# Kernel tuning notes

Measured on AMD Instinct MI355X. Metric: run time of the kernel, lower is better.

## Reference

```python
import jax, jax.numpy as jnp
import numpy as np

N, E, G = 100000, 1600000, 512
D_IN, D_H, D_OUT = 128, 128, 1
EPS = 1e-5


def _gcn_conv(x, W, b, src, dst, n):
    # PyG GCNConv: h = x @ W, add self-loops, symmetric-normalized sum aggregation, bias after.
    h = x @ W
    loop = jnp.arange(n)
    s = jnp.concatenate([src, loop])
    d = jnp.concatenate([dst, loop])
    deg = jax.ops.segment_sum(jnp.ones(s.shape[0], dtype=h.dtype), d, num_segments=n)
    dinv = jnp.where(deg > 0, jax.lax.rsqrt(deg), 0.0)
    norm = dinv[s] * dinv[d]  # [E+N]
    out = jax.ops.segment_sum(h[s] * norm[:, None], d, num_segments=n)
    return out + b


def _bn(x, g, b, m, v):
    # eval-mode BatchNorm1d
    return (x - m) * jax.lax.rsqrt(v + EPS) * g + b


def setup_inputs() -> dict:
    key = jax.random.key(0)
    ks = jax.random.split(key, 24)
    x = jax.random.normal(ks[0], (N, D_IN), dtype=jnp.float32)
    edge_index = jax.random.randint(ks[1], (2, E), 0, N, dtype=jnp.int64)
    batch = (jnp.arange(N, dtype=jnp.int64) * G) // N  # sorted, all graphs non-empty
    inp = {"x": x, "edge_index": edge_index, "batch": batch}
    dims = [(D_IN, D_H), (D_H, D_H), (D_H, D_H)]
    for i, (din, dout) in enumerate(dims):
        sc = 1.0 / np.sqrt(din)
        inp[f"W{i}"] = jax.random.normal(ks[2 + 4 * i], (din, dout), dtype=jnp.float32) * sc
        inp[f"cb{i}"] = jnp.zeros((dout,), dtype=jnp.float32)
        inp[f"g{i}"] = jnp.ones((dout,), dtype=jnp.float32)
        inp[f"bt{i}"] = jnp.zeros((dout,), dtype=jnp.float32)
        inp[f"m{i}"] = jax.random.normal(ks[3 + 4 * i], (dout,), dtype=jnp.float32) * 0.1
        inp[f"v{i}"] = jax.random.uniform(ks[4 + 4 * i], (dout,), dtype=jnp.float32, minval=0.5, maxval=1.5)
    inp["L1w"] = jax.random.normal(ks[15], (2 * D_H, D_H), dtype=jnp.float32) / np.sqrt(2 * D_H)
    inp["L1b"] = jnp.zeros((D_H,), dtype=jnp.float32)
    inp["L2w"] = jax.random.normal(ks[16], (D_H, D_H // 2), dtype=jnp.float32) / np.sqrt(D_H)
    inp["L2b"] = jnp.zeros((D_H // 2,), dtype=jnp.float32)
    inp["L3w"] = jax.random.normal(ks[17], (D_H // 2, D_OUT), dtype=jnp.float32) / np.sqrt(D_H // 2)
    inp["L3b"] = jnp.zeros((D_OUT,), dtype=jnp.float32)
    return inp


def reference(x, edge_index, batch,
              W0, cb0, g0, bt0, m0, v0,
              W1, cb1, g1, bt1, m1, v1,
              W2, cb2, g2, bt2, m2, v2,
              L1w, L1b, L2w, L2b, L3w, L3b):
    src, dst = edge_index[0], edge_index[1]
    Ws = [W0, W1, W2]
    cbs = [cb0, cb1, cb2]
    bns = [(g0, bt0, m0, v0), (g1, bt1, m1, v1), (g2, bt2, m2, v2)]
    for i in range(3):
        x_prev = x
        x = _gcn_conv(x, Ws[i], cbs[i], src, dst, N)
        x = jax.nn.relu(_bn(x, *bns[i]))
        # dropout is identity in eval mode
        if i > 0:
            x = x + x_prev  # residual (shapes match for i > 0)
    ones = jnp.ones((N,), dtype=x.dtype)
    cnt = jax.ops.segment_sum(ones, batch, num_segments=G)[:, None]
    x_mean = jax.ops.segment_sum(x, batch, num_segments=G) / cnt
    x_max = jax.ops.segment_max(x, batch, num_segments=G)
    h = jnp.concatenate([x_mean, x_max], axis=1)  # [G, 2*D_H]
    h = jax.nn.relu(h @ L1w + L1b)
    h = jax.nn.relu(h @ L2w + L2b)
    return h @ L3w + L3b  # [G, 1]
```

## Files before the change

kernel.cpp:

```cpp
#include <hip/hip_runtime.h>
#include <math.h>

#define DH 128
#define EPSB 1e-5f
#define MAXB 832
#define BCAP 2560
#define LDAP 136

typedef __attribute__((ext_vector_type(8))) short short8;
typedef __attribute__((ext_vector_type(4))) float f32x4;

static __device__ __forceinline__ unsigned short f2bf(float f) {
    unsigned u = __float_as_uint(f);
    u += 0x7fffu + ((u >> 16) & 1u);
    return (unsigned short)(u >> 16);
}
static __device__ __forceinline__ float bf2f(unsigned short h) {
    return __uint_as_float(((unsigned)h) << 16);
}
static __device__ __forceinline__ float blo(unsigned u) { return __uint_as_float(u << 16); }
static __device__ __forceinline__ float bhi(unsigned u) { return __uint_as_float(u & 0xFFFF0000u); }


__launch_bounds__(256)
__global__ void k_bucketA(const int* __restrict__ src, const int* __restrict__ dst,
                          int* __restrict__ gcur, int* __restrict__ bbuf,
                          const int* __restrict__ batch, int* __restrict__ starts,
                          const float* __restrict__ W0, const float* __restrict__ W1,
                          const float* __restrict__ W2, unsigned short* __restrict__ Wf0,
                          int E, int NB, int chunk, int N, int G)
{
    const int t = threadIdx.x;

    if (blockIdx.x >= 512) {
        int fid = (blockIdx.x - 512) * 4 + (t >> 6);
        int lane = t & 63;
        int l = fid >> 6, f = fid & 63;
        const float* W = (l == 0) ? W0 : (l == 1) ? W1 : W2;
        unsigned short* Wf = Wf0 + (size_t)l * 32768;
        int nt = f & 3, s = (f >> 2) & 3, p = (f >> 4) & 1, nh = f >> 5;
        int n = nh * 64 + nt * 16 + (lane & 15);
        int kbase = s * 32 + (lane >> 4) * 8;
        unsigned short o[8];
#pragma unroll
        for (int j = 0; j < 8; ++j) {
            float w = W[(size_t)(kbase + j) * DH + n];
            unsigned short h = f2bf(w);
            o[j] = p ? f2bf(w - bf2f(h)) : h;
        }
        unsigned short* d = Wf + (size_t)f * 512 + lane * 8;
        *(ushort4*)d       = make_ushort4(o[0], o[1], o[2], o[3]);
        *(ushort4*)(d + 4) = make_ushort4(o[4], o[5], o[6], o[7]);
        return;
    }

    __shared__ int cnt[MAXB];
    __shared__ int base[MAXB];

    for (int i = blockIdx.x * 256 + t; i < N; i += 512 * 256) {
        int b = batch[i];
        if (i == 0) { starts[0] = 0; starts[G] = N; }
        else if (batch[i - 1] != b) starts[b] = i;
    }

    for (int i = t; i < NB; i += 256) cnt[i] = 0;
    __syncthreads();
    const int e0 = blockIdx.x * chunk;
    const int e1 = min(E, e0 + chunk);
    for (int e = e0 + t; e < e1; e += 256)
        atomicAdd(&cnt[dst[e] >> 7], 1);
    __syncthreads();
    for (int i = t; i < NB; i += 256) {
        int c = cnt[i];
        base[i] = (c > 0) ? atomicAdd(&gcur[i], c) : 0;
        cnt[i] = 0;
    }
    __syncthreads();
    for (int e = e0 + t; e < e1; e += 256) {
        int d = dst[e];
        int b = d >> 7;
        int o = base[b] + atomicAdd(&cnt[b], 1);
        if (o < BCAP) bbuf[(size_t)b * BCAP + o] = (src[e] << 7) | (d & 127);
    }
}


__launch_bounds__(256)
__global__ void k_bfinal(const int* __restrict__ gcur, int* __restrict__ bbuf,
                         int2* __restrict__ rowinfo, float* __restrict__ dinv, int N)
{
    __shared__ int ebuf[BCAP];
    __shared__ int dcnt[128];
    __shared__ int sp[128];
    const int b = blockIdx.x, t = threadIdx.x;
    const int c = min(gcur[b], BCAP);
    const int base = b * BCAP;
    int* p = bbuf + base;
    for (int i = t; i < c; i += 256) ebuf[i] = p[i];
    if (t < 128) dcnt[t] = 0;
    __syncthreads();
    for (int i = t; i < c; i += 256) atomicAdd(&dcnt[ebuf[i] & 127], 1);
    __syncthreads();
    if (t < 128) sp[t] = dcnt[t];
    __syncthreads();
    for (int off = 1; off < 128; off <<= 1) {
        int u = (t < 128 && t >= off) ? sp[t - off] : 0;
        __syncthreads();
        if (t < 128) sp[t] += u;
        __syncthreads();
    }
    if (t < 128) {
        sp[t] -= dcnt[t];
        int d = b * 128 + t;
        if (d < N) {
            rowinfo[d] = make_int2(base + sp[t], base + sp[t] + dcnt[t]);
            dinv[d] = rsqrtf((float)(dcnt[t] + 1));
        }
        dcnt[t] = 0;
    }
    __syncthreads();
    for (int i = t; i < c; i += 256) {
        int e = ebuf[i];
        int dl = e & 127;
        int o = atomicAdd(&dcnt[dl], 1);
        p[sp[dl] + o] = e >> 7;
    }
}


__launch_bounds__(256)
__global__ void k_gemm0(const float* __restrict__ X,
                        const unsigned short* __restrict__ Wf,
                        const float* __restrict__ dinv,
                        unsigned short* __restrict__ hs, int N)
{
    __shared__ unsigned short Ah[16 * 512];
    __shared__ unsigned short Al[16 * 512];

    const int tid  = threadIdx.x;
    const int lane = tid & 63, wave = tid >> 6;
    const int mh = wave >> 1, nh = wave & 1;
    const int rowBase = blockIdx.x * 64;
    const int r15 = lane & 15, quad = lane >> 4;

    {
        const int gl = tid >> 4;
        const int f8 = (tid & 15) * 8;
        const int s  = f8 >> 5;
        const int q  = (f8 >> 3) & 3;
        const int lp = q * 16 + gl;
#pragma unroll
        for (int it = 0; it < 4; ++it) {
            int row = rowBase + it * 16 + gl;
            float v[8];
            if (row < N) {
                float4 a0 = *(const float4*)(X + (size_t)row * DH + f8);
                float4 a1 = *(const float4*)(X + (size_t)row * DH + f8 + 4);
                v[0] = a0.x; v[1] = a0.y; v[2] = a0.z; v[3] = a0.w;
                v[4] = a1.x; v[5] = a1.y; v[6] = a1.z; v[7] = a1.w;
            } else {
#pragma unroll
                for (int j = 0; j < 8; ++j) v[j] = 0.f;
            }
            unsigned short hA[8], lA[8];
#pragma unroll
            for (int j = 0; j < 8; ++j) {
                unsigned short h = f2bf(v[j]);
                hA[j] = h; lA[j] = f2bf(v[j] - bf2f(h));
            }
            int reg = it * 4 + s;
            *(ushort4*)(Ah + reg * 512 + lp * 8)     = make_ushort4(hA[0], hA[1], hA[2], hA[3]);
            *(ushort4*)(Ah + reg * 512 + lp * 8 + 4) = make_ushort4(hA[4], hA[5], hA[6], hA[7]);
            *(ushort4*)(Al + reg * 512 + lp * 8)     = make_ushort4(lA[0], lA[1], lA[2], lA[3]);
            *(ushort4*)(Al + reg * 512 + lp * 8 + 4) = make_ushort4(lA[4], lA[5], lA[6], lA[7]);
        }
    }
    __syncthreads();

    f32x4 acc[2][4];
#pragma unroll
    for (int mt = 0; mt < 2; ++mt)
#pragma unroll
        for (int nt = 0; nt < 4; ++nt)
            acc[mt][nt] = (f32x4){0.f, 0.f, 0.f, 0.f};

#pragma unroll
    for (int s = 0; s < 4; ++s) {
        short8 wfh[4], wfl[4];
#pragma unroll
        for (int nt = 0; nt < 4; ++nt) {
            wfh[nt] = *(const short8*)(Wf + ((((nh * 2 + 0) * 4 + s) * 4 + nt) * 512) + lane * 8);
            wfl[nt] = *(const short8*)(Wf + ((((nh * 2 + 1) * 4 + s) * 4 + nt) * 512) + lane * 8);
        }
#pragma unroll
        for (int mt = 0; mt < 2; ++mt) {
            int reg = (mh * 2 + mt) * 4 + s;
            short8 ah = *(const short8*)(Ah + reg * 512 + lane * 8);
            short8 al = *(const short8*)(Al + reg * 512 + lane * 8);
#pragma unroll
            for (int nt = 0; nt < 4; ++nt) {
                acc[mt][nt] = __builtin_amdgcn_mfma_f32_16x16x32_bf16(ah, wfh[nt], acc[mt][nt], 0, 0, 0);
                acc[mt][nt] = __builtin_amdgcn_mfma_f32_16x16x32_bf16(ah, wfl[nt], acc[mt][nt], 0, 0, 0);
                acc[mt][nt] = __builtin_amdgcn_mfma_f32_16x16x32_bf16(al, wfh[nt], acc[mt][nt], 0, 0, 0);
            }
        }
    }

#pragma unroll
    for (int mt = 0; mt < 2; ++mt) {
        int rl = mh * 32 + mt * 16 + quad * 4;
#pragma unroll
        for (int reg = 0; reg < 4; ++reg) {
            int row = rowBase + rl + reg;
            if (row < N) {
                float sc = dinv[row];
#pragma unroll
                for (int nt = 0; nt < 4; ++nt)
                    hs[(size_t)row * DH + nh * 64 + nt * 16 + r15] = f2bf(acc[mt][nt][reg] * sc);
            }
        }
    }
}


__launch_bounds__(256)
__global__ void k_gather_mm(const unsigned short* __restrict__ hs,
                            const int2* __restrict__ rowinfo,
                            const int* __restrict__ csr_src,
                            const float* __restrict__ dinv,
                            const float* __restrict__ cb, const float* __restrict__ bm,
                            const float* __restrict__ bv, const float* __restrict__ bg,
                            const float* __restrict__ bb,
                            const float* __restrict__ prev,
                            float* __restrict__ feat,
                            const unsigned short* __restrict__ Wf,
                            unsigned short* __restrict__ hs_next,
                            int N)
{
    __shared__ unsigned short Ah[16 * LDAP];
    __shared__ unsigned short Al[16 * LDAP];

    const int tid = threadIdx.x;
    const int nb = tid >> 4, lh = tid & 15;
    const int nodeBase = blockIdx.x * 16;
    const int node = nodeBase + nb;
    const int f = lh * 8;

    if (node < N) {
        int2 ri = rowinfo[node];
        const uint4* hsv = (const uint4*)hs;
        float a[8];
        {
            uint4 sv = hsv[(size_t)node * 16 + lh];
            a[0] = blo(sv.x); a[1] = bhi(sv.x); a[2] = blo(sv.y); a[3] = bhi(sv.y);
            a[4] = blo(sv.z); a[5] = bhi(sv.z); a[6] = blo(sv.w); a[7] = bhi(sv.w);
        }
        for (int base = ri.x; base < ri.y; base += 16) {
            int cnt = ri.y - base; if (cnt > 16) cnt = 16;
            int idx = (lh < cnt) ? csr_src[base + lh] : 0;
            int i = 0;
            for (; i + 4 <= cnt; i += 4) {
                int s0 = __shfl(idx, i,     16), s1 = __shfl(idx, i + 1, 16);
                int s2 = __shfl(idx, i + 2, 16), s3 = __shfl(idx, i + 3, 16);
                uint4 v0 = hsv[(size_t)s0 * 16 + lh];
                uint4 v1 = hsv[(size_t)s1 * 16 + lh];
                uint4 v2 = hsv[(size_t)s2 * 16 + lh];
                uint4 v3 = hsv[(size_t)s3 * 16 + lh];
                a[0] += (blo(v0.x) + blo(v1.x)) + (blo(v2.x) + blo(v3.x));
                a[1] += (bhi(v0.x) + bhi(v1.x)) + (bhi(v2.x) + bhi(v3.x));
                a[2] += (blo(v0.y) + blo(v1.y)) + (blo(v2.y) + blo(v3.y));
                a[3] += (bhi(v0.y) + bhi(v1.y)) + (bhi(v2.y) + bhi(v3.y));
                a[4] += (blo(v0.z) + blo(v1.z)) + (blo(v2.z) + blo(v3.z));
                a[5] += (bhi(v0.z) + bhi(v1.z)) + (bhi(v2.z) + bhi(v3.z));
                a[6] += (blo(v0.w) + blo(v1.w)) + (blo(v2.w) + blo(v3.w));
                a[7] += (bhi(v0.w) + bhi(v1.w)) + (bhi(v2.w) + bhi(v3.w));
            }
            for (; i < cnt; ++i) {
                int s = __shfl(idx, i, 16);
                uint4 v = hsv[(size_t)s * 16 + lh];
                a[0] += blo(v.x); a[1] += bhi(v.x); a[2] += blo(v.y); a[3] += bhi(v.y);
                a[4] += blo(v.z); a[5] += bhi(v.z); a[6] += blo(v.w); a[7] += bhi(v.w);
            }
        }

        const float sc = dinv[node];
        float cbv[8], bmv[8], bvv[8], bgv[8], bbv[8];
        *(float4*)cbv = *(const float4*)(cb + f); *(float4*)(cbv + 4) = *(const float4*)(cb + f + 4);
        *(float4*)bmv = *(const float4*)(bm + f); *(float4*)(bmv + 4) = *(const float4*)(bm + f + 4);
        *(float4*)bvv = *(const float4*)(bv + f); *(float4*)(bvv + 4) = *(const float4*)(bv + f + 4);
        *(float4*)bgv = *(const float4*)(bg + f); *(float4*)(bgv + 4) = *(const float4*)(bg + f + 4);
        *(float4*)bbv = *(const float4*)(bb + f); *(float4*)(bbv + 4) = *(const float4*)(bb + f + 4);

        float o[8];
#pragma unroll
        for (int j = 0; j < 8; ++j) {
            float v = (a[j] * sc + cbv[j] - bmv[j]) * rsqrtf(bvv[j] + EPSB) * bgv[j] + bbv[j];
            o[j] = fmaxf(v, 0.f);
        }
        if (prev) {
            float4 p0 = *(const float4*)(prev + (size_t)node * DH + f);
            float4 p1 = *(const float4*)(prev + (size_t)node * DH + f + 4);
            o[0] += p0.x; o[1] += p0.y; o[2] += p0.z; o[3] += p0.w;
            o[4] += p1.x; o[5] += p1.y; o[6] += p1.z; o[7] += p1.w;
        }
        *(float4*)(feat + (size_t)node * DH + f)     = make_float4(o[0], o[1], o[2], o[3]);
        *(float4*)(feat + (size_t)node * DH + f + 4) = make_float4(o[4], o[5], o[6], o[7]);

        unsigned short hA[8], lA[8];
#pragma unroll
        for (int j = 0; j < 8; ++j) {
            unsigned short h = f2bf(o[j]);
            hA[j] = h; lA[j] = f2bf(o[j] - bf2f(h));
        }
        *(ushort4*)(Ah + nb * LDAP + f)     = make_ushort4(hA[0], hA[1], hA[2], hA[3]);
        *(ushort4*)(Ah + nb * LDAP + f + 4) = make_ushort4(hA[4], hA[5], hA[6], hA[7]);
        *(ushort4*)(Al + nb * LDAP + f)     = make_ushort4(lA[0], lA[1], lA[2], lA[3]);
        *(ushort4*)(Al + nb * LDAP + f + 4) = make_ushort4(lA[4], lA[5], lA[6], lA[7]);
    }
    __syncthreads();

    const int lane = tid & 63, wave = tid >> 6;
    const int r15 = lane & 15, quad = lane >> 4;

    f32x4 acc[2];
    acc[0] = (f32x4){0.f, 0.f, 0.f, 0.f};
    acc[1] = (f32x4){0.f, 0.f, 0.f, 0.f};

#pragma unroll
    for (int s = 0; s < 4; ++s) {
        short8 ah = *(const short8*)(Ah + r15 * LDAP + s * 32 + quad * 8);
        short8 al = *(const short8*)(Al + r15 * LDAP + s * 32 + quad * 8);
#pragma unroll
        for (int j = 0; j < 2; ++j) {
            int ntg = wave * 2 + j;
            int nh = ntg >> 2, nt = ntg & 3;
            short8 wh = *(const short8*)(Wf + ((((nh * 2 + 0) * 4 + s) * 4 + nt) * 512) + lane * 8);
            short8 wl = *(const short8*)(Wf + ((((nh * 2 + 1) * 4 + s) * 4 + nt) * 512) + lane * 8);
            acc[j] = __builtin_amdgcn_mfma_f32_16x16x32_bf16(ah, wh, acc[j], 0, 0, 0);
            acc[j] = __builtin_amdgcn_mfma_f32_16x16x32_bf16(ah, wl, acc[j], 0, 0, 0);
            acc[j] = __builtin_amdgcn_mfma_f32_16x16x32_bf16(al, wh, acc[j], 0, 0, 0);
        }
    }

    float dv[4];
#pragma unroll
    for (int reg = 0; reg < 4; ++reg) {
        int row = nodeBase + quad * 4 + reg;
        dv[reg] = (row < N) ? dinv[row] : 0.f;
    }
#pragma unroll
    for (int j = 0; j < 2; ++j) {
        int col = (wave * 2 + j) * 16 + r15;
#pragma unroll
        for (int reg = 0; reg < 4; ++reg) {
            int row = nodeBase + quad * 4 + reg;
            if (row < N)
                hs_next[(size_t)row * DH + col] = f2bf(acc[j][reg] * dv[reg]);
        }
    }
}


__launch_bounds__(256)
__global__ void k_gather_pool(const unsigned short* __restrict__ hs,
                              const int2* __restrict__ rowinfo,
                              const int* __restrict__ csr_src,
                              const float* __restrict__ dinv,
                              const float* __restrict__ cb, const float* __restrict__ bm,
                              const float* __restrict__ bv, const float* __restrict__ bg,
                              const float* __restrict__ bb,
                              const float* __restrict__ prev,
                              const int* __restrict__ batch,
                              float* __restrict__ sumAcc,
                              unsigned* __restrict__ maxAcc,
                              int N)
{
    __shared__ float fsh[16][128];
    __shared__ float psum[2][2][128];
    __shared__ float pmax[2][2][128];
    __shared__ int   sb[16];

    const int tid = threadIdx.x;
    const int nb = tid >> 4, lh = tid & 15;
    const int nodeBase = blockIdx.x * 16;
    const int node = nodeBase + nb;
    const int f = lh * 8;

    const int g0 = batch[nodeBase];
    const int g1 = batch[min(nodeBase + 15, N - 1)];

    if (tid < 16) {
        int nn = nodeBase + tid;
        sb[tid] = (nn < N && batch[nn] != g0) ? 1 : 0;
    }
    if (nodeBase + 16 > N) {
        if (node >= N) {
#pragma unroll
            for (int j = 0; j < 8; ++j) fsh[nb][f + j] = 0.f;
        }
    }

    if (node < N) {
        int2 ri = rowinfo[node];
        const uint4* hsv = (const uint4*)hs;
        float a[8];
        {
            uint4 sv = hsv[(size_t)node * 16 + lh];
            a[0] = blo(sv.x); a[1] = bhi(sv.x); a[2] = blo(sv.y); a[3] = bhi(sv.y);
            a[4] = blo(sv.z); a[5] = bhi(sv.z); a[6] = blo(sv.w); a[7] = bhi(sv.w);
        }
        for (int base = ri.x; base < ri.y; base += 16) {
            int cnt = ri.y - base; if (cnt > 16) cnt = 16;
            int idx = (lh < cnt) ? csr_src[base + lh] : 0;
            int i = 0;
            for (; i + 4 <= cnt; i += 4) {
                int s0 = __shfl(idx, i,     16), s1 = __shfl(idx, i + 1, 16);
                int s2 = __shfl(idx, i + 2, 16), s3 = __shfl(idx, i + 3, 16);
                uint4 v0 = hsv[(size_t)s0 * 16 + lh];
                uint4 v1 = hsv[(size_t)s1 * 16 + lh];
                uint4 v2 = hsv[(size_t)s2 * 16 + lh];
                uint4 v3 = hsv[(size_t)s3 * 16 + lh];
                a[0] += (blo(v0.x) + blo(v1.x)) + (blo(v2.x) + blo(v3.x));
                a[1] += (bhi(v0.x) + bhi(v1.x)) + (bhi(v2.x) + bhi(v3.x));
                a[2] += (blo(v0.y) + blo(v1.y)) + (blo(v2.y) + blo(v3.y));
                a[3] += (bhi(v0.y) + bhi(v1.y)) + (bhi(v2.y) + bhi(v3.y));
                a[4] += (blo(v0.z) + blo(v1.z)) + (blo(v2.z) + blo(v3.z));
                a[5] += (bhi(v0.z) + bhi(v1.z)) + (bhi(v2.z) + bhi(v3.z));
                a[6] += (blo(v0.w) + blo(v1.w)) + (blo(v2.w) + blo(v3.w));
                a[7] += (bhi(v0.w) + bhi(v1.w)) + (bhi(v2.w) + bhi(v3.w));
            }
            for (; i < cnt; ++i) {
                int s = __shfl(idx, i, 16);
                uint4 v = hsv[(size_t)s * 16 + lh];
                a[0] += blo(v.x); a[1] += bhi(v.x); a[2] += blo(v.y); a[3] += bhi(v.y);
                a[4] += blo(v.z); a[5] += bhi(v.z); a[6] += blo(v.w); a[7] += bhi(v.w);
            }
        }

        const float sc = dinv[node];
        float cbv[8], bmv[8], bvv[8], bgv[8], bbv[8];
        *(float4*)cbv = *(const float4*)(cb + f); *(float4*)(cbv + 4) = *(const float4*)(cb + f + 4);
        *(float4*)bmv = *(const float4*)(bm + f); *(float4*)(bmv + 4) = *(const float4*)(bm + f + 4);
        *(float4*)bvv = *(const float4*)(bv + f); *(float4*)(bvv + 4) = *(const float4*)(bv + f + 4);
        *(float4*)bgv = *(const float4*)(bg + f); *(float4*)(bgv + 4) = *(const float4*)(bg + f + 4);
        *(float4*)bbv = *(const float4*)(bb + f); *(float4*)(bbv + 4) = *(const float4*)(bb + f + 4);

        float4 p0 = *(const float4*)(prev + (size_t)node * DH + f);
        float4 p1 = *(const float4*)(prev + (size_t)node * DH + f + 4);
        float o[8];
#pragma unroll
        for (int j = 0; j < 8; ++j) {
            float v = (a[j] * sc + cbv[j] - bmv[j]) * rsqrtf(bvv[j] + EPSB) * bgv[j] + bbv[j];
            o[j] = fmaxf(v, 0.f);
        }
        o[0] += p0.x; o[1] += p0.y; o[2] += p0.z; o[3] += p0.w;
        o[4] += p1.x; o[5] += p1.y; o[6] += p1.z; o[7] += p1.w;

        *(float4*)(&fsh[nb][f])     = make_float4(o[0], o[1], o[2], o[3]);
        *(float4*)(&fsh[nb][f + 4]) = make_float4(o[4], o[5], o[6], o[7]);
    }
    __syncthreads();

    const int half = tid >> 7;
    const int fi = tid & 127;
    float s0 = 0.f, s1 = 0.f, m0 = 0.f, m1 = 0.f;
#pragma unroll
    for (int r = 0; r < 8; ++r) {
        int row = half * 8 + r;
        float v = fsh[row][fi];
        if (sb[row]) { s1 += v; m1 = fmaxf(m1, v); }
        else         { s0 += v; m0 = fmaxf(m0, v); }
    }
    psum[half][0][fi] = s0; psum[half][1][fi] = s1;
    pmax[half][0][fi] = m0; pmax[half][1][fi] = m1;
    __syncthreads();

    if (half == 0) {
        float ts0 = psum[0][0][fi] + psum[1][0][fi];
        float tm0 = fmaxf(pmax[0][0][fi], pmax[1][0][fi]);
        unsafeAtomicAdd(&sumAcc[(size_t)g0 * 128 + fi], ts0);
        atomicMax(&maxAcc[(size_t)g0 * 128 + fi], __float_as_uint(tm0));
        if (g1 != g0) {
            float ts1 = psum[0][1][fi] + psum[1][1][fi];
            float tm1 = fmaxf(pmax[0][1][fi], pmax[1][1][fi]);
            unsafeAtomicAdd(&sumAcc[(size_t)g1 * 128 + fi], ts1);
            atomicMax(&maxAcc[(size_t)g1 * 128 + fi], __float_as_uint(tm1));
        }
    }
}


__launch_bounds__(128)
__global__ void k_head(const float* __restrict__ sumAcc, const unsigned* __restrict__ maxAcc,
                       const int* __restrict__ starts,
                       const float* __restrict__ L1w, const float* __restrict__ L1b,
                       const float* __restrict__ L2w, const float* __restrict__ L2b,
                       const float* __restrict__ L3w, const float* __restrict__ L3b,
                       float* __restrict__ out)
{
    int g = blockIdx.x, t = threadIdx.x;
    float cnt = (float)(starts[g + 1] - starts[g]);

    __shared__ float h[256];
    h[t]       = sumAcc[(size_t)g * 128 + t] / cnt;
    h[128 + t] = __uint_as_float(maxAcc[(size_t)g * 128 + t]);
    __syncthreads();

    float a = L1b[t];
    for (int k = 0; k < 256; ++k) a += h[k] * L1w[k * DH + t];
    __shared__ float h1[128];
    h1[t] = fmaxf(a, 0.f);
    __syncthreads();

    __shared__ float h2[64];
    if (t < 64) {
        float a2 = L2b[t];
        for (int k = 0; k < 128; ++k) a2 += h1[k] * L2w[k * 64 + t];
        h2[t] = fmaxf(a2, 0.f);
    }
    __syncthreads();

    if (t < 64) {
        float p = h2[t] * L3w[t];
#pragma unroll
        for (int off = 32; off > 0; off >>= 1) p += __shfl_down(p, off, 64);
        if (t == 0) out[g] = p + L3b[0];
    }
}


static inline char* align16(char* p) {
    return (char*)(((uintptr_t)p + 15) & ~(uintptr_t)15);
}

extern "C" void kernel_launch(void* const* d_in, const int* in_sizes, int n_in,
                              void* d_out, int out_size, void* d_ws, size_t ws_size,
                              hipStream_t stream)
{
    const float* x     = (const float*)d_in[0];
    const int*   ei    = (const int*)d_in[1];
    const int*   batch = (const int*)d_in[2];
    const int N = in_sizes[0] / DH;
    const int E = in_sizes[1] / 2;
    const int G = out_size;
    const int* src = ei;
    const int* dst = ei + E;

    const float* W[3]  = {(const float*)d_in[3],  (const float*)d_in[9],  (const float*)d_in[15]};
    const float* cb[3] = {(const float*)d_in[4],  (const float*)d_in[10], (const float*)d_in[16]};
    const float* bg[3] = {(const float*)d_in[5],  (const float*)d_in[11], (const float*)d_in[17]};
    const float* bt[3] = {(const float*)d_in[6],  (const float*)d_in[12], (const float*)d_in[18]};
    const float* bm[3] = {(const float*)d_in[7],  (const float*)d_in[13], (const float*)d_in[19]};
    const float* bv[3] = {(const float*)d_in[8],  (const float*)d_in[14], (const float*)d_in[20]};
    const float* L1w = (const float*)d_in[21]; const float* L1b = (const float*)d_in[22];
    const float* L2w = (const float*)d_in[23]; const float* L2b = (const float*)d_in[24];
    const float* L3w = (const float*)d_in[25]; const float* L3b = (const float*)d_in[26];

    char* wsp = (char*)d_ws;
    size_t featB = (size_t)N * DH * sizeof(float);
    size_t hsB   = (size_t)N * DH * sizeof(unsigned short);
    float* F_A = (float*)wsp; wsp += featB;
    float* F_B = (float*)wsp; wsp += featB;
    unsigned short* HS0 = (unsigned short*)F_B;
    unsigned short* HS1 = (unsigned short*)wsp; wsp += hsB;
    unsigned short* HS2 = (unsigned short*)wsp; wsp += hsB;
    unsigned short* Wfrag = (unsigned short*)wsp; wsp += 3 * 65536;
    int2*  rowinfo = (int2*)wsp;  wsp += (size_t)N * sizeof(int2);
    float* dinv    = (float*)wsp; wsp += (size_t)N * sizeof(float);
    int*   starts  = (int*)wsp;   wsp = align16(wsp + (size_t)(G + 1) * sizeof(int));
    int*      gcur   = (int*)wsp;      wsp += (size_t)MAXB * sizeof(int);
    float*    sumAcc = (float*)wsp;    wsp += (size_t)G * 128 * sizeof(float);
    unsigned* maxAcc = (unsigned*)wsp; wsp += (size_t)G * 128 * sizeof(unsigned);
    size_t zeroBytes = (size_t)MAXB * sizeof(int) + (size_t)G * 128 * 8;
    int*   bbuf    = (int*)align16(wsp); wsp = (char*)bbuf + (size_t)MAXB * BCAP * sizeof(int);

    const int NB = (N + 127) >> 7;
    const int nblkA = 512;
    const int chunk = (E + nblkA - 1) / nblkA;

    hipMemsetAsync(gcur, 0, zeroBytes, stream);
    k_bucketA<<<nblkA + 48, 256, 0, stream>>>(src, dst, gcur, bbuf, batch, starts,
                                              W[0], W[1], W[2], Wfrag,
                                              E, NB, chunk, N, G);
    k_bfinal <<<NB, 256, 0, stream>>>(gcur, bbuf, rowinfo, dinv, N);

    int gemmGrid = (N + 63) / 64;
    int gathGrid = (N + 15) / 16;

    k_gemm0<<<gemmGrid, 256, 0, stream>>>(x, Wfrag, dinv, HS0, N);
    k_gather_mm<<<gathGrid, 256, 0, stream>>>(HS0, rowinfo, bbuf, dinv,
                                              cb[0], bm[0], bv[0], bg[0], bt[0],
                                              nullptr, F_A, Wfrag + 32768, HS1, N);
    k_gather_mm<<<gathGrid, 256, 0, stream>>>(HS1, rowinfo, bbuf, dinv,
                                              cb[1], bm[1], bv[1], bg[1], bt[1],
                                              F_A, F_B, Wfrag + 65536, HS2, N);
    k_gather_pool<<<gathGrid, 256, 0, stream>>>(HS2, rowinfo, bbuf, dinv,
                                                cb[2], bm[2], bv[2], bg[2], bt[2],
                                                F_B, batch, sumAcc, maxAcc, N);

    k_head<<<G, 128, 0, stream>>>(sumAcc, maxAcc, starts,
                                  L1w, L1b, L2w, L2b, L3w, L3b, (float*)d_out);
}
```

Baseline: 466.6 us.

## Merge bucket finalize with first GEMM and apply source-degree scaling in gather

Drops the source-side dinv prescale from the GEMM epilogues, so the first GEMM no longer depends on the bucket-finalize results. The two then run as one launch with disjoint block ranges. To keep the maths the same, the gather kernels load dinv for each source index, broadcast it by shuffle and multiply each neighbor row by it. This saves one kernel launch and lets the two stages overlap, at the cost of extra per-edge dinv loads and multiplies in every gather layer.

```diff
diff --git a/kernel.cpp b/kernel.cpp
--- a/kernel.cpp
+++ b/kernel.cpp
@@ -86,66 +86,67 @@
 
 
 __launch_bounds__(256)
-__global__ void k_bfinal(const int* __restrict__ gcur, int* __restrict__ bbuf,
-                         int2* __restrict__ rowinfo, float* __restrict__ dinv, int N)
+__global__ void k_bf_gemm0(const int* __restrict__ gcur, int* __restrict__ bbuf,
+                           int2* __restrict__ rowinfo, float* __restrict__ dinv,
+                           const float* __restrict__ X,
+                           const unsigned short* __restrict__ Wf,
+                           unsigned short* __restrict__ hs,
+                           int N, int NB)
 {
-    __shared__ int ebuf[BCAP];
-    __shared__ int dcnt[128];
-    __shared__ int sp[128];
-    const int b = blockIdx.x, t = threadIdx.x;
-    const int c = min(gcur[b], BCAP);
-    const int base = b * BCAP;
-    int* p = bbuf + base;
-    for (int i = t; i < c; i += 256) ebuf[i] = p[i];
-    if (t < 128) dcnt[t] = 0;
-    __syncthreads();
-    for (int i = t; i < c; i += 256) atomicAdd(&dcnt[ebuf[i] & 127], 1);
-    __syncthreads();
-    if (t < 128) sp[t] = dcnt[t];
-    __syncthreads();
-    for (int off = 1; off < 128; off <<= 1) {
-        int u = (t < 128 && t >= off) ? sp[t - off] : 0;
+    __shared__ __align__(16) unsigned char smem[32768];
+    const int t = threadIdx.x;
+
+    if (blockIdx.x < NB) {
+        int* ebuf = (int*)smem;
+        int* dcnt = (int*)(smem + 10240);
+        int* sp   = (int*)(smem + 10752);
+        const int b = blockIdx.x;
+        const int c = min(gcur[b], BCAP);
+        const int base = b * BCAP;
+        int* p = bbuf + base;
+        for (int i = t; i < c; i += 256) ebuf[i] = p[i];
+        if (t < 128) dcnt[t] = 0;
         __syncthreads();
-        if (t < 128) sp[t] += u;
+        for (int i = t; i < c; i += 256) atomicAdd(&dcnt[ebuf[i] & 127], 1);
         __syncthreads();
-    }
-    if (t < 128) {
-        sp[t] -= dcnt[t];
-        int d = b * 128 + t;
-        if (d < N) {
-            rowinfo[d] = make_int2(base + sp[t], base + sp[t] + dcnt[t]);
-            dinv[d] = rsqrtf((float)(dcnt[t] + 1));
-        }
-        dcnt[t] = 0;
-    }
-    __syncthreads();
-    for (int i = t; i < c; i += 256) {
-        int e = ebuf[i];
-        int dl = e & 127;
-        int o = atomicAdd(&dcnt[dl], 1);
-        p[sp[dl] + o] = e >> 7;
-    }
-}
-
-
-__launch_bounds__(256)
-__global__ void k_gemm0(const float* __restrict__ X,
-                        const unsigned short* __restrict__ Wf,
-                        const float* __restrict__ dinv,
-                        unsigned short* __restrict__ hs, int N)
-{
-    __shared__ unsigned short Ah[16 * 512];
-    __shared__ unsigned short Al[16 * 512];
-
-    const int tid  = threadIdx.x;
-    const int lane = tid & 63, wave = tid >> 6;
+        if (t < 128) sp[t] = dcnt[t];
+        __syncthreads();
+        for (int off = 1; off < 128; off <<= 1) {
+            int u = (t < 128 && t >= off) ? sp[t - off] : 0;
+            __syncthreads();
+            if (t < 128) sp[t] += u;
+            __syncthreads();
+        }
+        if (t < 128) {
+            sp[t] -= dcnt[t];
+            int d = b * 128 + t;
+            if (d < N) {
+                rowinfo[d] = make_int2(base + sp[t], base + sp[t] + dcnt[t]);
+                dinv[d] = rsqrtf((float)(dcnt[t] + 1));
+            }
+            dcnt[t] = 0;
+        }
+        __syncthreads();
+        for (int i = t; i < c; i += 256) {
+            int e = ebuf[i];
+            int dl = e & 127;
+            int o = atomicAdd(&dcnt[dl], 1);
+            p[sp[dl] + o] = e >> 7;
+        }
+        return;
+    }
+
+    unsigned short* Ah = (unsigned short*)smem;
+    unsigned short* Al = (unsigned short*)(smem + 16384);
+
+    const int lane = t & 63, wave = t >> 6;
     const int mh = wave >> 1, nh = wave & 1;
-    const int rowBase = blockIdx.x * 64;
+    const int rowBase = (blockIdx.x - NB) * 64;
     const int r15 = lane & 15, quad = lane >> 4;
 
     {
-        const int gl = tid >> 4;
-        const int f8 = (tid & 15) * 8;
+        const int gl = t >> 4;
+        const int f8 = (t & 15) * 8;
         const int s  = f8 >> 5;
         const int q  = (f8 >> 3) & 3;
         const int lp = q * 16 + gl;
@@ -213,10 +214,9 @@
         for (int reg = 0; reg < 4; ++reg) {
             int row = rowBase + rl + reg;
             if (row < N) {
-                float sc = dinv[row];
 #pragma unroll
                 for (int nt = 0; nt < 4; ++nt)
-                    hs[(size_t)row * DH + nh * 64 + nt * 16 + r15] = f2bf(acc[mt][nt][reg] * sc);
+                    hs[(size_t)row * DH + nh * 64 + nt * 16 + r15] = f2bf(acc[mt][nt][reg]);
             }
         }
     }
@@ -248,42 +248,50 @@
 
     if (node < N) {
         int2 ri = rowinfo[node];
+        const float dn = dinv[node];
         const uint4* hsv = (const uint4*)hs;
         float a[8];
         {
             uint4 sv = hsv[(size_t)node * 16 + lh];
-            a[0] = blo(sv.x); a[1] = bhi(sv.x); a[2] = blo(sv.y); a[3] = bhi(sv.y);
-            a[4] = blo(sv.z); a[5] = bhi(sv.z); a[6] = blo(sv.w); a[7] = bhi(sv.w);
+            a[0] = dn * blo(sv.x); a[1] = dn * bhi(sv.x);
+            a[2] = dn * blo(sv.y); a[3] = dn * bhi(sv.y);
+            a[4] = dn * blo(sv.z); a[5] = dn * bhi(sv.z);
+            a[6] = dn * blo(sv.w); a[7] = dn * bhi(sv.w);
         }
         for (int base = ri.x; base < ri.y; base += 16) {
             int cnt = ri.y - base; if (cnt > 16) cnt = 16;
             int idx = (lh < cnt) ? csr_src[base + lh] : 0;
+            float dvl = dinv[idx];
             int i = 0;
             for (; i + 4 <= cnt; i += 4) {
                 int s0 = __shfl(idx, i,     16), s1 = __shfl(idx, i + 1, 16);
                 int s2 = __shfl(idx, i + 2, 16), s3 = __shfl(idx, i + 3, 16);
+                float d0 = __shfl(dvl, i,     16), d1 = __shfl(dvl, i + 1, 16);
+                float d2 = __shfl(dvl, i + 2, 16), d3 = __shfl(dvl, i + 3, 16);
                 uint4 v0 = hsv[(size_t)s0 * 16 + lh];
                 uint4 v1 = hsv[(size_t)s1 * 16 + lh];
                 uint4 v2 = hsv[(size_t)s2 * 16 + lh];
                 uint4 v3 = hsv[(size_t)s3 * 16 + lh];
-                a[0] += (blo(v0.x) + blo(v1.x)) + (blo(v2.x) + blo(v3.x));
-                a[1] += (bhi(v0.x) + bhi(v1.x)) + (bhi(v2.x) + bhi(v3.x));
-                a[2] += (blo(v0.y) + blo(v1.y)) + (blo(v2.y) + blo(v3.y));
-                a[3] += (bhi(v0.y) + bhi(v1.y)) + (bhi(v2.y) + bhi(v3.y));
-                a[4] += (blo(v0.z) + blo(v1.z)) + (blo(v2.z) + blo(v3.z));
-                a[5] += (bhi(v0.z) + bhi(v1.z)) + (bhi(v2.z) + bhi(v3.z));
-                a[6] += (blo(v0.w) + blo(v1.w)) + (blo(v2.w) + blo(v3.w));
-                a[7] += (bhi(v0.w) + bhi(v1.w)) + (bhi(v2.w) + bhi(v3.w));
+                a[0] += (d0 * blo(v0.x) + d1 * blo(v1.x)) + (d2 * blo(v2.x) + d3 * blo(v3.x));
+                a[1] += (d0 * bhi(v0.x) + d1 * bhi(v1.x)) + (d2 * bhi(v2.x) + d3 * bhi(v3.x));
+                a[2] += (d0 * blo(v0.y) + d1 * blo(v1.y)) + (d2 * blo(v2.y) + d3 * blo(v3.y));
+                a[3] += (d0 * bhi(v0.y) + d1 * bhi(v1.y)) + (d2 * bhi(v2.y) + d3 * bhi(v3.y));
+                a[4] += (d0 * blo(v0.z) + d1 * blo(v1.z)) + (d2 * blo(v2.z) + d3 * blo(v3.z));
+                a[5] += (d0 * bhi(v0.z) + d1 * bhi(v1.z)) + (d2 * bhi(v2.z) + d3 * bhi(v3.z));
+                a[6] += (d0 * blo(v0.w) + d1 * blo(v1.w)) + (d2 * blo(v2.w) + d3 * blo(v3.w));
+                a[7] += (d0 * bhi(v0.w) + d1 * bhi(v1.w)) + (d2 * bhi(v2.w) + d3 * bhi(v3.w));
             }
             for (; i < cnt; ++i) {
                 int s = __shfl(idx, i, 16);
+                float dd = __shfl(dvl, i, 16);
                 uint4 v = hsv[(size_t)s * 16 + lh];
-                a[0] += blo(v.x); a[1] += bhi(v.x); a[2] += blo(v.y); a[3] += bhi(v.y);
-                a[4] += blo(v.z); a[5] += bhi(v.z); a[6] += blo(v.w); a[7] += bhi(v.w);
-            }
-        }
-
-        const float sc = dinv[node];
+                a[0] += dd * blo(v.x); a[1] += dd * bhi(v.x);
+                a[2] += dd * blo(v.y); a[3] += dd * bhi(v.y);
+                a[4] += dd * blo(v.z); a[5] += dd * bhi(v.z);
+                a[6] += dd * blo(v.w); a[7] += dd * bhi(v.w);
+            }
+        }
+
         float cbv[8], bmv[8], bvv[8], bgv[8], bbv[8];
         *(float4*)cbv = *(const float4*)(cb + f); *(float4*)(cbv + 4) = *(const float4*)(cb + f + 4);
         *(float4*)bmv = *(const float4*)(bm + f); *(float4*)(bmv + 4) = *(const float4*)(bm + f + 4);
@@ -294,7 +302,7 @@
         float o[8];
 #pragma unroll
         for (int j = 0; j < 8; ++j) {
-            float v = (a[j] * sc + cbv[j] - bmv[j]) * rsqrtf(bvv[j] + EPSB) * bgv[j] + bbv[j];
+            float v = (a[j] * dn + cbv[j] - bmv[j]) * rsqrtf(bvv[j] + EPSB) * bgv[j] + bbv[j];
             o[j] = fmaxf(v, 0.f);
         }
         if (prev) {
@@ -342,12 +350,6 @@
         }
     }
 
-    float dv[4];
-#pragma unroll
-    for (int reg = 0; reg < 4; ++reg) {
-        int row = nodeBase + quad * 4 + reg;
-        dv[reg] = (row < N) ? dinv[row] : 0.f;
-    }
 #pragma unroll
     for (int j = 0; j < 2; ++j) {
         int col = (wave * 2 + j) * 16 + r15;
@@ -355,7 +357,7 @@
         for (int reg = 0; reg < 4; ++reg) {
             int row = nodeBase + quad * 4 + reg;
             if (row < N)
-                hs_next[(size_t)row * DH + col] = f2bf(acc[j][reg] * dv[reg]);
+                hs_next[(size_t)row * DH + col] = f2bf(acc[j][reg]);
         }
     }
 }
@@ -402,42 +404,50 @@
 
     if (node < N) {
         int2 ri = rowinfo[node];
+        const float dn = dinv[node];
         const uint4* hsv = (const uint4*)hs;
         float a[8];
         {
             uint4 sv = hsv[(size_t)node * 16 + lh];
-            a[0] = blo(sv.x); a[1] = bhi(sv.x); a[2] = blo(sv.y); a[3] = bhi(sv.y);
-            a[4] = blo(sv.z); a[5] = bhi(sv.z); a[6] = blo(sv.w); a[7] = bhi(sv.w);
+            a[0] = dn * blo(sv.x); a[1] = dn * bhi(sv.x);
+            a[2] = dn * blo(sv.y); a[3] = dn * bhi(sv.y);
+            a[4] = dn * blo(sv.z); a[5] = dn * bhi(sv.z);
+            a[6] = dn * blo(sv.w); a[7] = dn * bhi(sv.w);
         }
         for (int base = ri.x; base < ri.y; base += 16) {
             int cnt = ri.y - base; if (cnt > 16) cnt = 16;
             int idx = (lh < cnt) ? csr_src[base + lh] : 0;
+            float dvl = dinv[idx];
             int i = 0;
             for (; i + 4 <= cnt; i += 4) {
                 int s0 = __shfl(idx, i,     16), s1 = __shfl(idx, i + 1, 16);
                 int s2 = __shfl(idx, i + 2, 16), s3 = __shfl(idx, i + 3, 16);
+                float d0 = __shfl(dvl, i,     16), d1 = __shfl(dvl, i + 1, 16);
+                float d2 = __shfl(dvl, i + 2, 16), d3 = __shfl(dvl, i + 3, 16);
                 uint4 v0 = hsv[(size_t)s0 * 16 + lh];
                 uint4 v1 = hsv[(size_t)s1 * 16 + lh];
                 uint4 v2 = hsv[(size_t)s2 * 16 + lh];
                 uint4 v3 = hsv[(size_t)s3 * 16 + lh];
-                a[0] += (blo(v0.x) + blo(v1.x)) + (blo(v2.x) + blo(v3.x));
-                a[1] += (bhi(v0.x) + bhi(v1.x)) + (bhi(v2.x) + bhi(v3.x));
-                a[2] += (blo(v0.y) + blo(v1.y)) + (blo(v2.y) + blo(v3.y));
-                a[3] += (bhi(v0.y) + bhi(v1.y)) + (bhi(v2.y) + bhi(v3.y));
-                a[4] += (blo(v0.z) + blo(v1.z)) + (blo(v2.z) + blo(v3.z));
-                a[5] += (bhi(v0.z) + bhi(v1.z)) + (bhi(v2.z) + bhi(v3.z));
-                a[6] += (blo(v0.w) + blo(v1.w)) + (blo(v2.w) + blo(v3.w));
-                a[7] += (bhi(v0.w) + bhi(v1.w)) + (bhi(v2.w) + bhi(v3.w));
+                a[0] += (d0 * blo(v0.x) + d1 * blo(v1.x)) + (d2 * blo(v2.x) + d3 * blo(v3.x));
+                a[1] += (d0 * bhi(v0.x) + d1 * bhi(v1.x)) + (d2 * bhi(v2.x) + d3 * bhi(v3.x));
+                a[2] += (d0 * blo(v0.y) + d1 * blo(v1.y)) + (d2 * blo(v2.y) + d3 * blo(v3.y));
+                a[3] += (d0 * bhi(v0.y) + d1 * bhi(v1.y)) + (d2 * bhi(v2.y) + d3 * bhi(v3.y));
+                a[4] += (d0 * blo(v0.z) + d1 * blo(v1.z)) + (d2 * blo(v2.z) + d3 * blo(v3.z));
+                a[5] += (d0 * bhi(v0.z) + d1 * bhi(v1.z)) + (d2 * bhi(v2.z) + d3 * bhi(v3.z));
+                a[6] += (d0 * blo(v0.w) + d1 * blo(v1.w)) + (d2 * blo(v2.w) + d3 * blo(v3.w));
+                a[7] += (d0 * bhi(v0.w) + d1 * bhi(v1.w)) + (d2 * bhi(v2.w) + d3 * bhi(v3.w));
             }
             for (; i < cnt; ++i) {
                 int s = __shfl(idx, i, 16);
+                float dd = __shfl(dvl, i, 16);
                 uint4 v = hsv[(size_t)s * 16 + lh];
-                a[0] += blo(v.x); a[1] += bhi(v.x); a[2] += blo(v.y); a[3] += bhi(v.y);
-                a[4] += blo(v.z); a[5] += bhi(v.z); a[6] += blo(v.w); a[7] += bhi(v.w);
-            }
-        }
-
-        const float sc = dinv[node];
+                a[0] += dd * blo(v.x); a[1] += dd * bhi(v.x);
+                a[2] += dd * blo(v.y); a[3] += dd * bhi(v.y);
+                a[4] += dd * blo(v.z); a[5] += dd * bhi(v.z);
+                a[6] += dd * blo(v.w); a[7] += dd * bhi(v.w);
+            }
+        }
+
         float cbv[8], bmv[8], bvv[8], bgv[8], bbv[8];
         *(float4*)cbv = *(const float4*)(cb + f); *(float4*)(cbv + 4) = *(const float4*)(cb + f + 4);
         *(float4*)bmv = *(const float4*)(bm + f); *(float4*)(bmv + 4) = *(const float4*)(bm + f + 4);
@@ -450,7 +460,7 @@
         float o[8];
 #pragma unroll
         for (int j = 0; j < 8; ++j) {
-            float v = (a[j] * sc + cbv[j] - bmv[j]) * rsqrtf(bvv[j] + EPSB) * bgv[j] + bbv[j];
+            float v = (a[j] * dn + cbv[j] - bmv[j]) * rsqrtf(bvv[j] + EPSB) * bgv[j] + bbv[j];
             o[j] = fmaxf(v, 0.f);
         }
         o[0] += p0.x; o[1] += p0.y; o[2] += p0.z; o[3] += p0.w;
@@ -577,17 +587,15 @@
     const int NB = (N + 127) >> 7;
     const int nblkA = 512;
     const int chunk = (E + nblkA - 1) / nblkA;
+    const int gemmGrid = (N + 63) / 64;
+    const int gathGrid = (N + 15) / 16;
 
     hipMemsetAsync(gcur, 0, zeroBytes, stream);
     k_bucketA<<<nblkA + 48, 256, 0, stream>>>(src, dst, gcur, bbuf, batch, starts,
                                               W[0], W[1], W[2], Wfrag,
                                               E, NB, chunk, N, G);
-    k_bfinal <<<NB, 256, 0, stream>>>(gcur, bbuf, rowinfo, dinv, N);
-
-    int gemmGrid = (N + 63) / 64;
-    int gathGrid = (N + 15) / 16;
-
-    k_gemm0<<<gemmGrid, 256, 0, stream>>>(x, Wfrag, dinv, HS0, N);
+    k_bf_gemm0<<<NB + gemmGrid, 256, 0, stream>>>(gcur, bbuf, rowinfo, dinv,
+                                                  x, Wfrag, HS0, N, NB);
     k_gather_mm<<<gathGrid, 256, 0, stream>>>(HS0, rowinfo, bbuf, dinv,
                                               cb[0], bm[0], bv[0], bg[0], bt[0],
                                               nullptr, F_A, Wfrag + 32768, HS1, N);
```

After: 453.6 us. 2.8% less time.
